# Performance work log

Hardware: AMD Instinct MI355X
Metric: run time of the kernel (lower is better)

Reference implementation:

```python
import jax, jax.numpy as jnp
import numpy as np

BN_EPS = 1e-5


def feature_gather(fmap, xy):
    """Bilinear grid_sample (align_corners=False, zero padding).
    fmap: (B, C, H, W), xy: (B, N, 2) in [-1, 1]. Returns (B, C, N)."""
    B, C, H, W = fmap.shape
    ix = ((xy[..., 0] + 1.0) * W - 1.0) * 0.5  # (B, N)
    iy = ((xy[..., 1] + 1.0) * H - 1.0) * 0.5
    ix0 = jnp.floor(ix); iy0 = jnp.floor(iy)
    ix1 = ix0 + 1.0;     iy1 = iy0 + 1.0
    wx1 = ix - ix0; wx0 = 1.0 - wx1
    wy1 = iy - iy0; wy0 = 1.0 - wy1

    def corner(fx, fy, w):
        valid = (fx >= 0) & (fx < W) & (fy >= 0) & (fy < H)
        xi = jnp.clip(fx, 0, W - 1).astype(jnp.int32)
        yi = jnp.clip(fy, 0, H - 1).astype(jnp.int32)
        # per-batch fancy gather: (C, H, W)[:, yi, xi] -> (C, N)
        vals = jax.vmap(lambda f, y, x: f[:, y, x])(fmap, yi, xi)  # (B, C, N)
        return vals * (w * valid.astype(fmap.dtype))[:, None, :]

    return (corner(ix0, iy0, wx0 * wy0) + corner(ix1, iy0, wx1 * wy0)
            + corner(ix0, iy1, wx0 * wy1) + corner(ix1, iy1, wx1 * wy1))


def bn1d(x, g, b, m, v):
    # x: (B, C, N); eval-mode batchnorm with running stats
    inv = jax.lax.rsqrt(v + BN_EPS)
    return (x - m[None, :, None]) * (g * inv)[None, :, None] + b[None, :, None]


def setup_inputs() -> dict:
    key = jax.random.key(0)
    ks = jax.random.split(key, 24)
    B, IC, PC, RC, OUT, H, W, N = 64, 32, 128, 32, 128, 96, 320, 2048
    s = 0.1
    return {
        "img_map": jax.random.normal(ks[0], (B, IC, H, W), jnp.float32),
        "xy": jax.random.uniform(ks[1], (B, N, 2), jnp.float32, -1.0, 1.0),
        "point_feas": jax.random.normal(ks[2], (B, PC, N), jnp.float32),
        "W_ia_conv": jax.random.normal(ks[3], (PC, IC), jnp.float32) * s,
        "b_ia_conv": jnp.zeros((PC,), jnp.float32),
        "g1": jnp.ones((PC,), jnp.float32),
        "bt1": jnp.zeros((PC,), jnp.float32),
        "m1": jax.random.normal(ks[4], (PC,), jnp.float32) * s,
        "v1": jax.random.uniform(ks[5], (PC,), jnp.float32, 0.5, 1.5),
        "Wf1": jax.random.normal(ks[6], (RC, IC), jnp.float32) * s,
        "bf1": jnp.zeros((RC,), jnp.float32),
        "Wf2": jax.random.normal(ks[7], (RC, PC), jnp.float32) * s,
        "bf2": jnp.zeros((RC,), jnp.float32),
        "Wf3": jax.random.normal(ks[8], (1, RC), jnp.float32) * s,
        "bf3": jnp.zeros((1,), jnp.float32),
        "W_fuse": jax.random.normal(ks[9], (OUT, 2 * PC), jnp.float32) * s,
        "b_fuse": jnp.zeros((OUT,), jnp.float32),
        "g2": jnp.ones((OUT,), jnp.float32),
        "bt2": jnp.zeros((OUT,), jnp.float32),
        "m2": jax.random.normal(ks[10], (OUT,), jnp.float32) * s,
        "v2": jax.random.uniform(ks[11], (OUT,), jnp.float32, 0.5, 1.5),
    }


def reference(img_map, xy, point_feas, W_ia_conv, b_ia_conv, g1, bt1, m1, v1,
              Wf1, bf1, Wf2, bf2, Wf3, bf3, W_fuse, b_fuse, g2, bt2, m2, v2):
    # Feature_Gather: sample image features at projected point locations
    img_feas = feature_gather(img_map, xy)  # (B, IC, N)

    # IA_Layer attention gate
    ri = jnp.einsum('bin,ri->brn', img_feas, Wf1) + bf1[None, :, None]
    rp = jnp.einsum('bpn,rp->brn', point_feas, Wf2) + bf2[None, :, None]
    att = jax.nn.sigmoid(jnp.einsum('brn,or->bon', jnp.tanh(ri + rp), Wf3)
                         + bf3[None, :, None])  # (B, 1, N)

    # IA_Layer conv1: 1x1 conv IC->PC + BN + ReLU, gated by attention
    img_new = jnp.einsum('bin,pi->bpn', img_feas, W_ia_conv) + b_ia_conv[None, :, None]
    img_new = jax.nn.relu(bn1d(img_new, g1, bt1, m1, v1)) * att  # (B, PC, N)

    # Atten_Fusion_Conv: concat + 1x1 conv + BN + ReLU
    fus = jnp.concatenate([point_feas, img_new], axis=1)  # (B, 2*PC, N)
    fus = jnp.einsum('bcn,oc->bon', fus, W_fuse) + b_fuse[None, :, None]
    return jax.nn.relu(bn1d(fus, g2, bt2, m2, v2))  # (B, OUT, N)
```

## Files before the change

kernel.cpp:

```cpp
#include <hip/hip_runtime.h>
#include <math.h>

typedef __attribute__((ext_vector_type(8))) short short8;
typedef __attribute__((ext_vector_type(4))) float floatx4;

constexpr int B    = 64;
constexpr int IC   = 32;
constexpr int PC   = 128;
constexpr int OUTC = 128;
constexpr int H    = 96;
constexpr int IW   = 320;
constexpr int NPT  = 2048;
constexpr float EPS = 1e-5f;

constexpr int BDIM = 256;
constexpr int NT   = 64;

__device__ __forceinline__ unsigned f2bf(float x) {
    unsigned u = __builtin_bit_cast(unsigned, x);
    u += 0x7FFFu + ((u >> 16) & 1u);
    return u >> 16;
}
__device__ __forceinline__ float fast_tanh(float v) {
    float e = __expf(2.f * v);
    return 1.f - 2.f / (e + 1.f);
}
__device__ __forceinline__ float fast_sigmoid(float v) {
    return 1.f / (1.f + __expf(-v));
}

__global__ __launch_bounds__(BDIM, 4) void rcnn_fused(
    const float* __restrict__ img_map, const float* __restrict__ xy,
    const float* __restrict__ point_feas,
    const float* __restrict__ Wia, const float* __restrict__ b_ia,
    const float* __restrict__ g1, const float* __restrict__ bt1,
    const float* __restrict__ m1, const float* __restrict__ v1,
    const float* __restrict__ Wf1, const float* __restrict__ bf1,
    const float* __restrict__ Wf2, const float* __restrict__ bf2,
    const float* __restrict__ Wf3, const float* __restrict__ bf3,
    const float* __restrict__ Wfuse, const float* __restrict__ b_fuse,
    const float* __restrict__ g2, const float* __restrict__ bt2,
    const float* __restrict__ m2, const float* __restrict__ v2,
    float* __restrict__ out)
{
    __shared__ __align__(16) short s_Ximg[NT][136];
    __shared__ __align__(16) char s_ovl[15360];
    __shared__ float s_sc[OUTC], s_bs[OUTC];

    short (*s_Wc)[40]  = (short(*)[40])s_ovl;
    short (*s_Xpf)[40] = (short(*)[40])(s_ovl + 10240);
    float (*s_if)[33]  = (float(*)[33])s_ovl;
    float (*s_attp)[NT]= (float(*)[NT])(s_ovl + 8448);

    const int t    = threadIdx.x;
    const int bid  = blockIdx.x;
    const int xcd  = bid & 7;
    const int rr   = bid >> 3;
    const int b    = (xcd << 3) | (rr >> 5);
    const int n0   = (rr & 31) * NT;
    const int lane = t & 63;
    const int w    = t >> 6;
    const int wq   = __builtin_amdgcn_readfirstlane(w);
    const int n    = n0 + lane;

    if (t < OUTC) {
        float sc = g2[t] * rsqrtf(v2[t] + EPS);
        s_sc[t] = sc;
        s_bs[t] = (b_fuse[t] - m2[t]) * sc + bt2[t];
    }

    {
        float xc = xy[((size_t)b * NPT + n) * 2 + 0];
        float yc = xy[((size_t)b * NPT + n) * 2 + 1];
        float ix = ((xc + 1.f) * (float)IW - 1.f) * 0.5f;
        float iy = ((yc + 1.f) * (float)H  - 1.f) * 0.5f;
        float fx0 = floorf(ix), fy0 = floorf(iy);
        float wx1 = ix - fx0, wx0f = 1.f - wx1;
        float wy1 = iy - fy0, wy0f = 1.f - wy1;
        int x0 = (int)fx0, y0 = (int)fy0;
        int x1 = x0 + 1,  y1 = y0 + 1;
        bool vx0 = (x0 >= 0) && (x0 < IW), vx1 = (x1 >= 0) && (x1 < IW);
        bool vy0 = (y0 >= 0) && (y0 < H),  vy1 = (y1 >= 0) && (y1 < H);
        int cx0 = min(max(x0, 0), IW - 1), cx1 = min(max(x1, 0), IW - 1);
        int cy0 = min(max(y0, 0), H - 1),  cy1 = min(max(y1, 0), H - 1);
        float w00 = wx0f * wy0f * ((vx0 && vy0) ? 1.f : 0.f);
        float w01 = wx1  * wy0f * ((vx1 && vy0) ? 1.f : 0.f);
        float w10 = wx0f * wy1  * ((vx0 && vy1) ? 1.f : 0.f);
        float w11 = wx1  * wy1  * ((vx1 && vy1) ? 1.f : 0.f);
        int o00 = cy0 * IW + cx0, o01 = cy0 * IW + cx1;
        int o10 = cy1 * IW + cx0, o11 = cy1 * IW + cx1;
        const float* fm = img_map + (size_t)b * IC * H * IW + (size_t)(wq * 8) * (H * IW);
        #pragma unroll
        for (int cc = 0; cc < 8; ++cc) {
            const float* f = fm + (size_t)cc * (H * IW);
            s_if[lane][wq * 8 + cc] = w00 * f[o00] + w01 * f[o01] + w10 * f[o10] + w11 * f[o11];
        }
    }
    __syncthreads();

    float fre[IC];
    #pragma unroll
    for (int c = 0; c < IC; ++c) fre[c] = s_if[lane][c];

    {
        float racc[8];
        #pragma unroll
        for (int i = 0; i < 8; ++i) racc[i] = bf1[wq * 8 + i] + bf2[wq * 8 + i];
        const float* pfb = point_feas + (size_t)b * PC * NPT + n;
        #pragma unroll 4
        for (int c = 0; c < PC; ++c) {
            float pf = pfb[(size_t)c * NPT];
            #pragma unroll
            for (int i = 0; i < 8; ++i)
                racc[i] += Wf2[(wq * 8 + i) * PC + c] * pf;
        }
        #pragma unroll
        for (int c = 0; c < IC; ++c) {
            #pragma unroll
            for (int i = 0; i < 8; ++i)
                racc[i] += Wf1[(wq * 8 + i) * IC + c] * fre[c];
        }
        float apart = 0.f;
        #pragma unroll
        for (int i = 0; i < 8; ++i) apart += Wf3[wq * 8 + i] * fast_tanh(racc[i]);
        s_attp[w][lane] = apart;
    }
    __syncthreads();

    {
        float att = fast_sigmoid(s_attp[0][lane] + s_attp[1][lane] + s_attp[2][lane]
                                 + s_attp[3][lane] + bf3[0]);
        #pragma unroll
        for (int jj = 0; jj < 4; ++jj) {
            short8 v;
            #pragma unroll
            for (int e = 0; e < 8; ++e) {
                int o = wq * 32 + jj * 8 + e;
                float acc = 0.f;
                #pragma unroll
                for (int c = 0; c < IC; ++c) acc += Wia[o * IC + c] * fre[c];
                float sc  = g1[o] * rsqrtf(v1[o] + EPS);
                float val = (acc + b_ia[o] - m1[o]) * sc + bt1[o];
                val = fmaxf(val, 0.f) * att;
                v[e] = (short)f2bf(val);
            }
            *(short8*)&s_Ximg[lane][wq * 32 + jj * 8] = v;
        }
    }
    __syncthreads();

    const int row16 = lane & 15;
    const int quad  = lane >> 4;
    floatx4 acc[2][4];
    #pragma unroll
    for (int mt = 0; mt < 2; ++mt)
        #pragma unroll
        for (int nt = 0; nt < 4; ++nt) acc[mt][nt] = (floatx4){0.f, 0.f, 0.f, 0.f};

    for (int chk = 0; chk < 8; ++chk) {
        const int k0 = chk * 32;
        #pragma unroll
        for (int j = 0; j < 8; ++j) {
            int idx = j * 256 + t;
            int c2 = (idx & 15) * 2, o = idx >> 4;
            float2 wv = *(const float2*)&Wfuse[o * 256 + k0 + c2];
            *(unsigned*)&s_Wc[o][c2] = f2bf(wv.x) | (f2bf(wv.y) << 16);
        }
        if (chk < 4) {
            #pragma unroll
            for (int j = 0; j < 4; ++j) {
                int idx = j * 256 + t;
                int n2 = (idx & 31) * 2, c = idx >> 5;
                float2 pv = *(const float2*)&point_feas[((size_t)b * PC + k0 + c) * NPT + n0 + n2];
                s_Xpf[n2][c]     = (short)f2bf(pv.x);
                s_Xpf[n2 + 1][c] = (short)f2bf(pv.y);
            }
        }
        __syncthreads();

        short8 afr[2], bfr[4];
        #pragma unroll
        for (int mt = 0; mt < 2; ++mt)
            afr[mt] = *(const short8*)&s_Wc[wq * 32 + mt * 16 + row16][quad * 8];
        #pragma unroll
        for (int nt = 0; nt < 4; ++nt) {
            const short* src = (chk < 4) ? &s_Xpf[nt * 16 + row16][quad * 8]
                                         : &s_Ximg[nt * 16 + row16][(chk - 4) * 32 + quad * 8];
            bfr[nt] = *(const short8*)src;
        }
        #pragma unroll
        for (int mt = 0; mt < 2; ++mt)
            #pragma unroll
            for (int nt = 0; nt < 4; ++nt)
                acc[mt][nt] = __builtin_amdgcn_mfma_f32_16x16x32_bf16(
                                  afr[mt], bfr[nt], acc[mt][nt], 0, 0, 0);
        if (chk != 7) __syncthreads();
    }

    #pragma unroll
    for (int mt = 0; mt < 2; ++mt) {
        #pragma unroll
        for (int nt = 0; nt < 4; ++nt) {
            #pragma unroll
            for (int r2 = 0; r2 < 4; ++r2) {
                int o = wq * 32 + mt * 16 + quad * 4 + r2;
                float val = fmaxf(acc[mt][nt][r2] * s_sc[o] + s_bs[o], 0.f);
                out[((size_t)b * OUTC + o) * NPT + n0 + nt * 16 + row16] = val;
            }
        }
    }
}

extern "C" void kernel_launch(void* const* d_in, const int* in_sizes, int n_in,
                              void* d_out, int out_size, void* d_ws, size_t ws_size,
                              hipStream_t stream) {
    const float* img_map    = (const float*)d_in[0];
    const float* xy         = (const float*)d_in[1];
    const float* point_feas = (const float*)d_in[2];
    const float* Wia        = (const float*)d_in[3];
    const float* b_ia       = (const float*)d_in[4];
    const float* g1         = (const float*)d_in[5];
    const float* bt1        = (const float*)d_in[6];
    const float* m1         = (const float*)d_in[7];
    const float* v1         = (const float*)d_in[8];
    const float* Wf1        = (const float*)d_in[9];
    const float* bf1        = (const float*)d_in[10];
    const float* Wf2        = (const float*)d_in[11];
    const float* bf2        = (const float*)d_in[12];
    const float* Wf3        = (const float*)d_in[13];
    const float* bf3        = (const float*)d_in[14];
    const float* Wfuse      = (const float*)d_in[15];
    const float* b_fuse     = (const float*)d_in[16];
    const float* g2         = (const float*)d_in[17];
    const float* bt2        = (const float*)d_in[18];
    const float* m2         = (const float*)d_in[19];
    const float* v2         = (const float*)d_in[20];
    float* out = (float*)d_out;

    rcnn_fused<<<dim3(2048), BDIM, 0, stream>>>(
        img_map, xy, point_feas, Wia, b_ia, g1, bt1, m1, v1,
        Wf1, bf1, Wf2, bf2, Wf3, bf3, Wfuse, b_fuse, g2, bt2, m2, v2, out);
}
```

Measured before the change: 567.9 us.

## Split fused kernel into prep kernel and larger-tile bf16 GEMM kernel

Splits the fused kernel into two. A prep kernel computes the gathered, attention-gated image features, converts point features to bf16, and writes a concatenated bf16 activation matrix plus bf16 fuse weights to the workspace. A second kernel then runs the fusion GEMM with 128x128 tiles per block, for better MFMA reuse and fewer barriers. The cost is an extra global write and read of the full intermediate activation matrix and a second launch. It falls back to the original fused kernel if the workspace is too small.

```diff
diff --git a/kernel.cpp b/kernel.cpp
--- a/kernel.cpp
+++ b/kernel.cpp
@@ -13,9 +13,6 @@
 constexpr int NPT  = 2048;
 constexpr float EPS = 1e-5f;
 
-constexpr int BDIM = 256;
-constexpr int NT   = 64;
-
 __device__ __forceinline__ unsigned f2bf(float x) {
     unsigned u = __builtin_bit_cast(unsigned, x);
     u += 0x7FFFu + ((u >> 16) & 1u);
@@ -29,7 +26,7 @@
     return 1.f / (1.f + __expf(-v));
 }
 
-__global__ __launch_bounds__(BDIM, 4) void rcnn_fused(
+__global__ __launch_bounds__(256, 4) void k1_prep(
     const float* __restrict__ img_map, const float* __restrict__ xy,
     const float* __restrict__ point_feas,
     const float* __restrict__ Wia, const float* __restrict__ b_ia,
@@ -38,35 +35,27 @@
     const float* __restrict__ Wf1, const float* __restrict__ bf1,
     const float* __restrict__ Wf2, const float* __restrict__ bf2,
     const float* __restrict__ Wf3, const float* __restrict__ bf3,
-    const float* __restrict__ Wfuse, const float* __restrict__ b_fuse,
-    const float* __restrict__ g2, const float* __restrict__ bt2,
-    const float* __restrict__ m2, const float* __restrict__ v2,
-    float* __restrict__ out)
+    const float* __restrict__ Wfuse,
+    short* __restrict__ Xg, short* __restrict__ Wb)
 {
-    __shared__ __align__(16) short s_Ximg[NT][136];
-    __shared__ __align__(16) char s_ovl[15360];
-    __shared__ float s_sc[OUTC], s_bs[OUTC];
-
-    short (*s_Wc)[40]  = (short(*)[40])s_ovl;
-    short (*s_Xpf)[40] = (short(*)[40])(s_ovl + 10240);
-    float (*s_if)[33]  = (float(*)[33])s_ovl;
-    float (*s_attp)[NT]= (float(*)[NT])(s_ovl + 8448);
-
-    const int t    = threadIdx.x;
-    const int bid  = blockIdx.x;
-    const int xcd  = bid & 7;
-    const int rr   = bid >> 3;
-    const int b    = (xcd << 3) | (rr >> 5);
-    const int n0   = (rr & 31) * NT;
-    const int lane = t & 63;
-    const int w    = t >> 6;
-    const int wq   = __builtin_amdgcn_readfirstlane(w);
-    const int n    = n0 + lane;
-
-    if (t < OUTC) {
-        float sc = g2[t] * rsqrtf(v2[t] + EPS);
-        s_sc[t] = sc;
-        s_bs[t] = (b_fuse[t] - m2[t]) * sc + bt2[t];
+    __shared__ float s_if[64][33];
+    __shared__ float s_attp[4][64];
+    __shared__ short s_Xpf[64 * 128];
+
+    const int t = threadIdx.x, bid = blockIdx.x;
+    const int xcd = bid & 7, rr = bid >> 3;
+    const int b  = (xcd << 3) | (rr >> 5);
+    const int n0 = (rr & 31) * 64;
+    const int lane = t & 63, w = t >> 6;
+    const int wq = __builtin_amdgcn_readfirstlane(w);
+    const int n = n0 + lane;
+
+    if (bid < 8) {
+        #pragma unroll
+        for (int j = 0; j < 16; ++j) {
+            int idx = bid * 4096 + j * 256 + t;
+            Wb[idx] = (short)f2bf(Wfuse[idx]);
+        }
     }
 
     {
@@ -102,6 +91,216 @@
     #pragma unroll
     for (int c = 0; c < IC; ++c) fre[c] = s_if[lane][c];
 
+    const float* pfb = point_feas + (size_t)b * PC * NPT + n;
+    {
+        float racc[8];
+        #pragma unroll
+        for (int i = 0; i < 8; ++i) racc[i] = bf1[wq * 8 + i] + bf2[wq * 8 + i];
+        #pragma unroll 4
+        for (int c = 0; c < PC; ++c) {
+            float pf = pfb[(size_t)c * NPT];
+            #pragma unroll
+            for (int i = 0; i < 8; ++i)
+                racc[i] += Wf2[(wq * 8 + i) * PC + c] * pf;
+        }
+        #pragma unroll
+        for (int c = 0; c < IC; ++c) {
+            #pragma unroll
+            for (int i = 0; i < 8; ++i)
+                racc[i] += Wf1[(wq * 8 + i) * IC + c] * fre[c];
+        }
+        float apart = 0.f;
+        #pragma unroll
+        for (int i = 0; i < 8; ++i) apart += Wf3[wq * 8 + i] * fast_tanh(racc[i]);
+        s_attp[w][lane] = apart;
+    }
+
+    #pragma unroll
+    for (int cc = 0; cc < 16; ++cc) {
+        int k0 = wq * 32 + cc * 2;
+        float a0 = pfb[(size_t)k0 * NPT];
+        float a1 = pfb[(size_t)(k0 + 1) * NPT];
+        unsigned pack = f2bf(a0) | (f2bf(a1) << 16);
+        int koct = k0 >> 3;
+        int sidx = lane * 128 + ((koct ^ (lane & 15)) << 3) + (k0 & 7);
+        *(unsigned*)&s_Xpf[sidx] = pack;
+    }
+    __syncthreads();
+
+    {
+        float att = fast_sigmoid(s_attp[0][lane] + s_attp[1][lane] + s_attp[2][lane]
+                                 + s_attp[3][lane] + bf3[0]);
+        #pragma unroll
+        for (int jj = 0; jj < 4; ++jj) {
+            short8 v;
+            #pragma unroll
+            for (int e = 0; e < 8; ++e) {
+                int o = wq * 32 + jj * 8 + e;
+                float acc = 0.f;
+                #pragma unroll
+                for (int c = 0; c < IC; ++c) acc += Wia[o * IC + c] * fre[c];
+                float sc  = g1[o] * rsqrtf(v1[o] + EPS);
+                float val = (acc + b_ia[o] - m1[o]) * sc + bt1[o];
+                val = fmaxf(val, 0.f) * att;
+                v[e] = (short)f2bf(val);
+            }
+            *(short8*)(Xg + ((size_t)(b * NPT + n)) * 256 + 128 + wq * 32 + jj * 8) = v;
+        }
+    }
+
+    #pragma unroll
+    for (int j = 0; j < 4; ++j) {
+        int idx = j * 256 + t;
+        int nn = idx >> 4, koct = idx & 15;
+        short8 v = *(const short8*)&s_Xpf[nn * 128 + ((koct ^ (nn & 15)) << 3)];
+        *(short8*)(Xg + ((size_t)(b * NPT + n0 + nn)) * 256 + koct * 8) = v;
+    }
+}
+
+__global__ __launch_bounds__(256, 4) void k2_gemm(
+    const short* __restrict__ Xg, const short* __restrict__ Wb,
+    const float* __restrict__ b_fuse, const float* __restrict__ g2,
+    const float* __restrict__ bt2, const float* __restrict__ m2,
+    const float* __restrict__ v2, float* __restrict__ out)
+{
+    __shared__ __align__(16) short sA[128][72];
+    __shared__ __align__(16) short sB[128][72];
+    __shared__ float s_sc[OUTC], s_bs[OUTC];
+
+    const int t = threadIdx.x;
+    const int b  = blockIdx.x >> 4;
+    const int n0 = (blockIdx.x & 15) * 128;
+    const int lane = t & 63, w = t >> 6;
+    const int wq = __builtin_amdgcn_readfirstlane(w);
+    const int mh = (wq & 1) * 64, nh = (wq >> 1) * 64;
+    const int r16 = lane & 15, quad = lane >> 4;
+
+    if (t < OUTC) {
+        float sc = g2[t] * rsqrtf(v2[t] + EPS);
+        s_sc[t] = sc;
+        s_bs[t] = (b_fuse[t] - m2[t]) * sc + bt2[t];
+    }
+
+    floatx4 acc[4][4];
+    #pragma unroll
+    for (int mt = 0; mt < 4; ++mt)
+        #pragma unroll
+        for (int nt = 0; nt < 4; ++nt) acc[mt][nt] = (floatx4){0.f, 0.f, 0.f, 0.f};
+
+    const short* Xrow = Xg + (size_t)(b * NPT + n0) * 256;
+
+    for (int kk = 0; kk < 4; ++kk) {
+        const int kb = kk * 64;
+        #pragma unroll
+        for (int j = 0; j < 4; ++j) {
+            int idx = j * 256 + t;
+            int m = idx >> 3, ko = idx & 7;
+            *(short8*)&sA[m][ko * 8] = *(const short8*)(Wb + m * 256 + kb + ko * 8);
+            *(short8*)&sB[m][ko * 8] = *(const short8*)(Xrow + (size_t)m * 256 + kb + ko * 8);
+        }
+        __syncthreads();
+
+        #pragma unroll
+        for (int kq = 0; kq < 2; ++kq) {
+            short8 af[4], bf[4];
+            #pragma unroll
+            for (int mt = 0; mt < 4; ++mt)
+                af[mt] = *(const short8*)&sA[mh + mt * 16 + r16][kq * 32 + quad * 8];
+            #pragma unroll
+            for (int nt = 0; nt < 4; ++nt)
+                bf[nt] = *(const short8*)&sB[nh + nt * 16 + r16][kq * 32 + quad * 8];
+            #pragma unroll
+            for (int mt = 0; mt < 4; ++mt)
+                #pragma unroll
+                for (int nt = 0; nt < 4; ++nt)
+                    acc[mt][nt] = __builtin_amdgcn_mfma_f32_16x16x32_bf16(
+                                      af[mt], bf[nt], acc[mt][nt], 0, 0, 0);
+        }
+        if (kk != 3) __syncthreads();
+    }
+
+    #pragma unroll
+    for (int mt = 0; mt < 4; ++mt) {
+        #pragma unroll
+        for (int nt = 0; nt < 4; ++nt) {
+            #pragma unroll
+            for (int r2 = 0; r2 < 4; ++r2) {
+                int o = mh + mt * 16 + quad * 4 + r2;
+                int nc = n0 + nh + nt * 16 + r16;
+                float val = fmaxf(acc[mt][nt][r2] * s_sc[o] + s_bs[o], 0.f);
+                out[((size_t)b * OUTC + o) * NPT + nc] = val;
+            }
+        }
+    }
+}
+
+__global__ __launch_bounds__(256, 4) void rcnn_fused(
+    const float* __restrict__ img_map, const float* __restrict__ xy,
+    const float* __restrict__ point_feas,
+    const float* __restrict__ Wia, const float* __restrict__ b_ia,
+    const float* __restrict__ g1, const float* __restrict__ bt1,
+    const float* __restrict__ m1, const float* __restrict__ v1,
+    const float* __restrict__ Wf1, const float* __restrict__ bf1,
+    const float* __restrict__ Wf2, const float* __restrict__ bf2,
+    const float* __restrict__ Wf3, const float* __restrict__ bf3,
+    const float* __restrict__ Wfuse, const float* __restrict__ b_fuse,
+    const float* __restrict__ g2, const float* __restrict__ bt2,
+    const float* __restrict__ m2, const float* __restrict__ v2,
+    float* __restrict__ out)
+{
+    __shared__ __align__(16) short s_Ximg[64][136];
+    __shared__ __align__(16) char s_ovl[15360];
+    __shared__ float s_sc[OUTC], s_bs[OUTC];
+
+    short (*s_Wc)[40]  = (short(*)[40])s_ovl;
+    short (*s_Xpf)[40] = (short(*)[40])(s_ovl + 10240);
+    float (*s_if)[33]  = (float(*)[33])s_ovl;
+    float (*s_attp)[64]= (float(*)[64])(s_ovl + 8448);
+
+    const int t = threadIdx.x, bid = blockIdx.x;
+    const int xcd = bid & 7, rr = bid >> 3;
+    const int b = (xcd << 3) | (rr >> 5);
+    const int n0 = (rr & 31) * 64;
+    const int lane = t & 63, w = t >> 6;
+    const int wq = __builtin_amdgcn_readfirstlane(w);
+    const int n = n0 + lane;
+
+    if (t < OUTC) {
+        float sc = g2[t] * rsqrtf(v2[t] + EPS);
+        s_sc[t] = sc;
+        s_bs[t] = (b_fuse[t] - m2[t]) * sc + bt2[t];
+    }
+    {
+        float xc = xy[((size_t)b * NPT + n) * 2 + 0];
+        float yc = xy[((size_t)b * NPT + n) * 2 + 1];
+        float ix = ((xc + 1.f) * (float)IW - 1.f) * 0.5f;
+        float iy = ((yc + 1.f) * (float)H  - 1.f) * 0.5f;
+        float fx0 = floorf(ix), fy0 = floorf(iy);
+        float wx1 = ix - fx0, wx0f = 1.f - wx1;
+        float wy1 = iy - fy0, wy0f = 1.f - wy1;
+        int x0 = (int)fx0, y0 = (int)fy0;
+        int x1 = x0 + 1,  y1 = y0 + 1;
+        bool vx0 = (x0 >= 0) && (x0 < IW), vx1 = (x1 >= 0) && (x1 < IW);
+        bool vy0 = (y0 >= 0) && (y0 < H),  vy1 = (y1 >= 0) && (y1 < H);
+        int cx0 = min(max(x0, 0), IW - 1), cx1 = min(max(x1, 0), IW - 1);
+        int cy0 = min(max(y0, 0), H - 1),  cy1 = min(max(y1, 0), H - 1);
+        float w00 = wx0f * wy0f * ((vx0 && vy0) ? 1.f : 0.f);
+        float w01 = wx1  * wy0f * ((vx1 && vy0) ? 1.f : 0.f);
+        float w10 = wx0f * wy1  * ((vx0 && vy1) ? 1.f : 0.f);
+        float w11 = wx1  * wy1  * ((vx1 && vy1) ? 1.f : 0.f);
+        int o00 = cy0 * IW + cx0, o01 = cy0 * IW + cx1;
+        int o10 = cy1 * IW + cx0, o11 = cy1 * IW + cx1;
+        const float* fm = img_map + (size_t)b * IC * H * IW + (size_t)(wq * 8) * (H * IW);
+        #pragma unroll
+        for (int cc = 0; cc < 8; ++cc) {
+            const float* f = fm + (size_t)cc * (H * IW);
+            s_if[lane][wq * 8 + cc] = w00 * f[o00] + w01 * f[o01] + w10 * f[o10] + w11 * f[o11];
+        }
+    }
+    __syncthreads();
+    float fre[IC];
+    #pragma unroll
+    for (int c = 0; c < IC; ++c) fre[c] = s_if[lane][c];
     {
         float racc[8];
         #pragma unroll
@@ -126,7 +325,6 @@
         s_attp[w][lane] = apart;
     }
     __syncthreads();
-
     {
         float att = fast_sigmoid(s_attp[0][lane] + s_attp[1][lane] + s_attp[2][lane]
                                  + s_attp[3][lane] + bf3[0]);
@@ -196,7 +394,6 @@
                                   afr[mt], bfr[nt], acc[mt][nt], 0, 0, 0);
         if (chk != 7) __syncthreads();
     }
-
     #pragma unroll
     for (int mt = 0; mt < 2; ++mt) {
         #pragma unroll
@@ -237,7 +434,18 @@
     const float* v2         = (const float*)d_in[20];
     float* out = (float*)d_out;
 
-    rcnn_fused<<<dim3(2048), BDIM, 0, stream>>>(
-        img_map, xy, point_feas, Wia, b_ia, g1, bt1, m1, v1,
-        Wf1, bf1, Wf2, bf2, Wf3, bf3, Wfuse, b_fuse, g2, bt2, m2, v2, out);
-}
+    const size_t need = 65536 + (size_t)B * NPT * 256 * 2;
+    if (ws_size >= need) {
+        short* Wb = (short*)d_ws;
+        short* Xg = (short*)((char*)d_ws + 65536);
+        k1_prep<<<dim3(2048), 256, 0, stream>>>(
+            img_map, xy, point_feas, Wia, b_ia, g1, bt1, m1, v1,
+            Wf1, bf1, Wf2, bf2, Wf3, bf3, Wfuse, Xg, Wb);
+        k2_gemm<<<dim3(1024), 256, 0, stream>>>(
+            Xg, Wb, b_fuse, g2, bt2, m2, v2, out);
+    } else {
+        rcnn_fused<<<dim3(2048), 256, 0, stream>>>(
+            img_map, xy, point_feas, Wia, b_ia, g1, bt1, m1, v1,
+            Wf1, bf1, Wf2, bf2, Wf3, bf3, Wfuse, b_fuse, g2, bt2, m2, v2, out);
+    }
+}
```

After: 547.4 us. 1.04x faster.
